# Optimization experiments

Measured on AMD Instinct MI355X. Metric: run time of the kernel, lower is better.

Reference implementation:

```python
import jax, jax.numpy as jnp
import numpy as np

N_NODES = 100000
N_EDGES = 1600000
HIDDEN = 128
N_GRAPHS = 64
N_CLASSES = 10


def setup_inputs() -> dict:
    key = jax.random.key(0)
    ks = jax.random.split(key, 10)
    x = jax.random.normal(ks[0], (N_NODES, 1), dtype=jnp.float32)
    edge_index = jax.random.randint(ks[1], (2, N_EDGES), 0, N_NODES, dtype=jnp.int32)
    batch = jnp.sort(jax.random.randint(ks[2], (N_NODES,), 0, N_GRAPHS, dtype=jnp.int32))
    def glorot(k, shape):
        fan_in, fan_out = shape
        s = jnp.sqrt(6.0 / (fan_in + fan_out))
        return jax.random.uniform(k, shape, jnp.float32, -s, s)
    return {
        "x": x,
        "edge_index": edge_index,
        "batch": batch,
        "W1l": glorot(ks[3], (1, HIDDEN)),
        "W1r": glorot(ks[4], (1, HIDDEN)),
        "b1": jnp.zeros((HIDDEN,), jnp.float32),
        "W2l": glorot(ks[5], (HIDDEN, HIDDEN)),
        "W2r": glorot(ks[6], (HIDDEN, HIDDEN)),
        "b2": jnp.zeros((HIDDEN,), jnp.float32),
        "W3l": glorot(ks[7], (HIDDEN, HIDDEN)),
        "W3r": glorot(ks[8], (HIDDEN, HIDDEN)),
        "b3": jnp.zeros((HIDDEN,), jnp.float32),
        "Wfc": glorot(ks[9], (HIDDEN, N_CLASSES)),
        "bfc": jnp.zeros((N_CLASSES,), jnp.float32),
    }


def _sage_conv(x, src, dst, Wl, Wr, b, n_nodes):
    # mean aggregation of source features at destination nodes
    msg = x[src]                                              # [E, d_in]
    agg = jax.ops.segment_sum(msg, dst, num_segments=n_nodes)  # [N, d_in]
    cnt = jax.ops.segment_sum(jnp.ones((src.shape[0], 1), x.dtype), dst,
                              num_segments=n_nodes)            # [N, 1]
    mean = agg / jnp.maximum(cnt, 1.0)
    # PyG SAGEConv: lin_l(mean neighbors) + bias + lin_r(self)
    return mean @ Wl + b + x @ Wr


def reference(x, edge_index, batch, W1l, W1r, b1, W2l, W2r, b2,
              W3l, W3r, b3, Wfc, bfc):
    src, dst = edge_index[0], edge_index[1]
    n = x.shape[0]
    h = jax.nn.relu(_sage_conv(x, src, dst, W1l, W1r, b1, n))
    h = jax.nn.relu(_sage_conv(h, src, dst, W2l, W2r, b2, n))
    h = jax.nn.relu(_sage_conv(h, src, dst, W3l, W3r, b3, n))
    # global_mean_pool over graph ids in `batch`
    pooled = jax.ops.segment_sum(h, batch, num_segments=N_GRAPHS)
    gcnt = jax.ops.segment_sum(jnp.ones((n, 1), h.dtype), batch,
                               num_segments=N_GRAPHS)
    pooled = pooled / jnp.maximum(gcnt, 1.0)
    logits = pooled @ Wfc + bfc
    return jax.nn.log_softmax(logits, axis=1)
```

## Files before the change

kernel.cpp:

```cpp
#include <hip/hip_runtime.h>

typedef unsigned int u32;
typedef unsigned short u16;
typedef short bf16x8 __attribute__((ext_vector_type(8)));
typedef float f32x4 __attribute__((ext_vector_type(4)));
typedef float f32x2 __attribute__((ext_vector_type(2)));
typedef u32 u32x4 __attribute__((ext_vector_type(4)));

#define HBLK 256

__device__ __forceinline__ u16 f2bf(float f) {
  u32 u = __float_as_uint(f);
  u = (u + 0x7FFFu + ((u >> 16) & 1u)) >> 16;
  return (u16)u;
}
__device__ __forceinline__ float bf2f(u32 h) { return __uint_as_float(h << 16); }

__global__ void hist_wprep_kernel(const int* __restrict__ dst, int* __restrict__ boff,
                                  int* __restrict__ btotal, int E, int nbuk, int chunk,
                                  const float* __restrict__ W2l, const float* __restrict__ W2r,
                                  const float* __restrict__ W3l, const float* __restrict__ W3r,
                                  u16* __restrict__ wt2, u16* __restrict__ wt3,
                                  float* __restrict__ pooled, int* __restrict__ gcnt) {
  int idx = blockIdx.x * 256 + threadIdx.x;
  {
    int which = idx >> 15, r = idx & 32767;
    int j = r >> 8, k = r & 255;
    if (which == 0) {
      float v = (k < 128) ? W2l[k * 128 + j] : W2r[(k - 128) * 128 + j];
      wt2[r] = f2bf(v);
    } else {
      float v = (k < 128) ? W3l[k * 128 + j] : W3r[(k - 128) * 128 + j];
      wt3[r] = f2bf(v);
    }
    if (idx < 8192) pooled[idx] = 0.f;
    if (idx < 64) gcnt[idx] = 0;
  }
  __shared__ int h[1024];
  for (int i = threadIdx.x; i < nbuk; i += 256) h[i] = 0;
  __syncthreads();
  int b0 = blockIdx.x * chunk, b1 = min(b0 + chunk, E);
  for (int e = b0 + threadIdx.x; e < b1; e += 256)
    atomicAdd(&h[dst[e] >> 7], 1);
  __syncthreads();
  for (int i = threadIdx.x; i < nbuk; i += 256)
    boff[i * HBLK + blockIdx.x] = atomicAdd(&btotal[i], h[i]);
}

__global__ void scatter2_kernel(const int* __restrict__ src, const int* __restrict__ dst,
                                const int* __restrict__ btotal, const int* __restrict__ boff,
                                u32* __restrict__ part, int* __restrict__ bbase,
                                int E, int nbuk, int chunk) {
  __shared__ int bt[1024];
  __shared__ int wsum[256];
  __shared__ int cur[1024];
  int tid = threadIdx.x;
  int t4 = tid * 4;
  int v0 = (t4 + 0 < nbuk) ? btotal[t4 + 0] : 0;
  int v1 = (t4 + 1 < nbuk) ? btotal[t4 + 1] : 0;
  int v2 = (t4 + 2 < nbuk) ? btotal[t4 + 2] : 0;
  int v3 = (t4 + 3 < nbuk) ? btotal[t4 + 3] : 0;
  int sum = v0 + v1 + v2 + v3;
  wsum[tid] = sum;
  __syncthreads();
  for (int off = 1; off < 256; off <<= 1) {
    int t = (tid >= off) ? wsum[tid - off] : 0;
    __syncthreads();
    wsum[tid] += t;
    __syncthreads();
  }
  int excl = wsum[tid] - sum;
  bt[t4 + 0] = excl;
  bt[t4 + 1] = excl + v0;
  bt[t4 + 2] = excl + v0 + v1;
  bt[t4 + 3] = excl + v0 + v1 + v2;
  __syncthreads();
  for (int i = tid; i < nbuk; i += 256) {
    cur[i] = bt[i] + boff[i * HBLK + blockIdx.x];
    if (blockIdx.x == 0) bbase[i] = bt[i];
  }
  __syncthreads();
  int b0 = blockIdx.x * chunk, b1 = min(b0 + chunk, E);
  for (int e = b0 + tid; e < b1; e += 256) {
    int d = dst[e];
    int pos = atomicAdd(&cur[d >> 7], 1);
    part[pos] = (u32)src[e] | ((u32)(d & 127) << 25);
  }
}

__global__ void scatter3_kernel(const u32* __restrict__ part, const int* __restrict__ bbase,
                                const float* __restrict__ x,
                                const float* __restrict__ W1l, const float* __restrict__ W1r,
                                const float* __restrict__ b1,
                                int* __restrict__ roff, int* __restrict__ csr,
                                u32* __restrict__ h1, int E, int nbuk, int n) {
  int b = blockIdx.x;
  int tid = threadIdx.x;
  int base = bbase[b];
  int end = (b + 1 < nbuk) ? bbase[b + 1] : E;
  __shared__ int cnt[128];
  __shared__ int s[128];
  __shared__ int cur[128];
  __shared__ float xsum[128];
  __shared__ float meanv[128];
  __shared__ float wlA[128], wrA[128], bA[128];
  if (tid < 128) {
    cnt[tid] = 0; xsum[tid] = 0.f;
    wlA[tid] = W1l[tid]; wrA[tid] = W1r[tid]; bA[tid] = b1[tid];
  }
  __syncthreads();
  for (int e = base + tid; e < end; e += 256)
    atomicAdd(&cnt[part[e] >> 25], 1);
  __syncthreads();
  if (tid < 128) s[tid] = cnt[tid];
  __syncthreads();
  for (int off = 1; off < 128; off <<= 1) {
    int t = (tid >= off && tid < 128) ? s[tid - off] : 0;
    __syncthreads();
    if (tid < 128) s[tid] += t;
    __syncthreads();
  }
  if (tid < 128) {
    int excl = s[tid] - cnt[tid];
    cur[tid] = base + excl;
    int node = b * 128 + tid;
    if (node < n) roff[node] = base + excl;
  }
  if (b == 0 && tid == 0) roff[n] = E;
  __syncthreads();
  for (int e = base + tid; e < end; e += 256) {
    u32 p = part[e];
    int sidx = (int)(p & 0x1FFFFFFu);
    int pos = atomicAdd(&cur[p >> 25], 1);
    csr[pos] = sidx;
    atomicAdd(&xsum[p >> 25], x[sidx]);
  }
  __syncthreads();
  if (tid < 128) meanv[tid] = xsum[tid] / (float)max(cnt[tid], 1);
  __syncthreads();
  int nlocal = min(128, n - b * 128);
  for (int q = tid; q < nlocal * 64; q += 256) {
    int ln = q >> 6, w = q & 63;
    int node = b * 128 + ln;
    int j0 = w * 2;
    float m = meanv[ln], xs = x[node];
    float v0 = fmaxf(m * wlA[j0] + xs * wrA[j0] + bA[j0], 0.f);
    float v1 = fmaxf(m * wlA[j0 + 1] + xs * wrA[j0 + 1] + bA[j0 + 1], 0.f);
    h1[(size_t)node * 64 + w] = (u32)f2bf(v0) | ((u32)f2bf(v1) << 16);
  }
}

__device__ __forceinline__ u32x4 grow(const u32* hp, int s) {
  return *(const u32x4*)(hp + (size_t)s * 64);
}
__device__ __forceinline__ void acc_row(f32x2* a, u32x4 v) {
#pragma unroll
  for (int w = 0; w < 4; ++w)
    a[w] += (f32x2){bf2f(v[w] & 0xFFFFu), bf2f(v[w] >> 16)};
}

__global__ void agg_kernel(const int* __restrict__ csr, const int* __restrict__ roff,
                           const u32* __restrict__ hin, u32* __restrict__ outv, int n) {
  int g = threadIdx.x >> 4, li = threadIdx.x & 15;
  int i = blockIdx.x * 16 + g;
  if (i >= n) return;
  int e0 = roff[i], e1 = roff[i + 1];
  f32x2 a[4] = {};
  const u32* hp = hin + li * 4;
  int e = e0;
  for (; e + 7 < e1; e += 8) {
    int s0 = csr[e], s1 = csr[e + 1], s2 = csr[e + 2], s3 = csr[e + 3];
    int s4 = csr[e + 4], s5 = csr[e + 5], s6 = csr[e + 6], s7 = csr[e + 7];
    u32x4 v0 = grow(hp, s0), v1 = grow(hp, s1), v2 = grow(hp, s2), v3 = grow(hp, s3);
    u32x4 v4 = grow(hp, s4), v5 = grow(hp, s5), v6 = grow(hp, s6), v7 = grow(hp, s7);
    acc_row(a, v0); acc_row(a, v1); acc_row(a, v2); acc_row(a, v3);
    acc_row(a, v4); acc_row(a, v5); acc_row(a, v6); acc_row(a, v7);
  }
  for (; e + 3 < e1; e += 4) {
    int s0 = csr[e], s1 = csr[e + 1], s2 = csr[e + 2], s3 = csr[e + 3];
    u32x4 v0 = grow(hp, s0), v1 = grow(hp, s1), v2 = grow(hp, s2), v3 = grow(hp, s3);
    acc_row(a, v0); acc_row(a, v1); acc_row(a, v2); acc_row(a, v3);
  }
  for (; e < e1; ++e) acc_row(a, grow(hp, csr[e]));
  float inv = 1.f / (float)max(e1 - e0, 1);
  u32x4 o;
#pragma unroll
  for (int w = 0; w < 4; ++w)
    o[w] = (u32)f2bf(a[w].x * inv) | ((u32)f2bf(a[w].y * inv) << 16);
  *(u32x4*)(outv + (size_t)i * 64 + li * 4) = o;
}

__launch_bounds__(512)
__global__ void mm_kernel(const u16* Aleft, const u16* Aright,
                          const u16* __restrict__ Wt, const float* __restrict__ bias,
                          u16* Out, int n) {
  __shared__ u16 wlds[32768];
  for (int c = threadIdx.x; c < 4096; c += 512) {
    int j = c >> 5, ch = c & 31;
    int swz = ch ^ (j & 31);
    *(u32x4*)(&wlds[j * 256 + swz * 8]) = *(const u32x4*)(&Wt[j * 256 + ch * 8]);
  }
  __syncthreads();
  int wave = threadIdx.x >> 6;
  int lane = threadIdx.x & 63;
  int quad = lane >> 4, l16 = lane & 15;
  int row0 = blockIdx.x * 128 + wave * 16;
  int m = row0 + l16;
  int mc = m < n ? m : (n - 1);
  f32x4 acc[8] = {};
  const u16* Ah[2] = {Aleft, Aright};
#pragma unroll
  for (int half = 0; half < 2; ++half) {
    const u16* A = Ah[half] + (size_t)mc * 128;
#pragma unroll
    for (int s = 0; s < 4; ++s) {
      bf16x8 a = *(const bf16x8*)(A + s * 32 + quad * 8);
      int chunk = (half << 4) + (s << 2) + quad;
#pragma unroll
      for (int t = 0; t < 8; ++t) {
        int j = t * 16 + l16;
        int swz = chunk ^ (j & 31);
        bf16x8 b = *(const bf16x8*)(&wlds[j * 256 + swz * 8]);
        acc[t] = __builtin_amdgcn_mfma_f32_16x16x32_bf16(a, b, acc[t], 0, 0, 0);
      }
    }
  }
  __syncthreads();
  int rl_base = wave * 16 + quad * 4;
#pragma unroll
  for (int t = 0; t < 8; ++t) {
    int j = t * 16 + l16;
    float bj = bias[j];
#pragma unroll
    for (int r = 0; r < 4; ++r) {
      float v = acc[t][r] + bj;
      wlds[(rl_base + r) * 136 + j] = f2bf(fmaxf(v, 0.f));
    }
  }
  __syncthreads();
  int base_row = blockIdx.x * 128;
  for (int q = 0; q < 4; ++q) {
    int idx = q * 512 + threadIdx.x;
    int rl = idx >> 4;
    int ch = idx & 15;
    int mr = base_row + rl;
    if (mr < n)
      *(u32x4*)(&Out[(size_t)mr * 128 + ch * 8]) =
          *(const u32x4*)(&wlds[rl * 136 + ch * 8]);
  }
}

#define PB_NODES 128
__global__ void pool_partial(const int* __restrict__ batch, const u32* __restrict__ h3,
                             float* __restrict__ pooled, int* __restrict__ gcnt, int n) {
  __shared__ int bg[PB_NODES];
  int tid = threadIdx.x;
  int start = blockIdx.x * PB_NODES;
  int cntN = min(PB_NODES, n - start);
  if (tid < cntN) bg[tid] = batch[start + tid];
  __syncthreads();
  int wave = tid >> 6, lane = tid & 63;
  float a0 = 0.f, a1 = 0.f;
  int gcur = -1, cnt = 0;
  int k = wave;
  for (; k + 12 < cntN; k += 16) {
    u32 v0 = h3[(size_t)(start + k) * 64 + lane];
    u32 v1 = h3[(size_t)(start + k + 4) * 64 + lane];
    u32 v2 = h3[(size_t)(start + k + 8) * 64 + lane];
    u32 v3 = h3[(size_t)(start + k + 12) * 64 + lane];
    int g0 = bg[k], g1 = bg[k + 4], g2 = bg[k + 8], g3 = bg[k + 12];
    u32 vv[4] = {v0, v1, v2, v3};
    int gg[4] = {g0, g1, g2, g3};
#pragma unroll
    for (int q = 0; q < 4; ++q) {
      if (gg[q] != gcur) {
        if (gcur >= 0) {
          atomicAdd(&pooled[gcur * 128 + lane * 2], a0);
          atomicAdd(&pooled[gcur * 128 + lane * 2 + 1], a1);
          if (lane == 0) atomicAdd(&gcnt[gcur], cnt);
        }
        gcur = gg[q]; a0 = 0.f; a1 = 0.f; cnt = 0;
      }
      a0 += bf2f(vv[q] & 0xFFFFu);
      a1 += bf2f(vv[q] >> 16);
      cnt++;
    }
  }
  for (; k < cntN; k += 4) {
    u32 v = h3[(size_t)(start + k) * 64 + lane];
    int g = bg[k];
    if (g != gcur) {
      if (gcur >= 0) {
        atomicAdd(&pooled[gcur * 128 + lane * 2], a0);
        atomicAdd(&pooled[gcur * 128 + lane * 2 + 1], a1);
        if (lane == 0) atomicAdd(&gcnt[gcur], cnt);
      }
      gcur = g; a0 = 0.f; a1 = 0.f; cnt = 0;
    }
    a0 += bf2f(v & 0xFFFFu);
    a1 += bf2f(v >> 16);
    cnt++;
  }
  if (gcur >= 0) {
    atomicAdd(&pooled[gcur * 128 + lane * 2], a0);
    atomicAdd(&pooled[gcur * 128 + lane * 2 + 1], a1);
    if (lane == 0) atomicAdd(&gcnt[gcur], cnt);
  }
}

__global__ void head_kernel(const float* __restrict__ pooled, const int* __restrict__ gcnt,
                            const float* __restrict__ Wfc, const float* __restrict__ bfc,
                            float* __restrict__ out) {
  __shared__ float lg[64][10];
  int t = threadIdx.x;
  if (t < 640) {
    int g = t / 10, c = t % 10;
    float inv = 1.f / (float)max(gcnt[g], 1);
    float acc = bfc[c];
    for (int k = 0; k < 128; ++k) acc += pooled[g * 128 + k] * inv * Wfc[k * 10 + c];
    lg[g][c] = acc;
  }
  __syncthreads();
  if (t < 640) {
    int g = t / 10, c = t % 10;
    float mx = -1e30f;
    for (int q = 0; q < 10; ++q) mx = fmaxf(mx, lg[g][q]);
    float se = 0.f;
    for (int q = 0; q < 10; ++q) se += expf(lg[g][q] - mx);
    out[g * 10 + c] = lg[g][c] - mx - logf(se);
  }
}

extern "C" void kernel_launch(void* const* d_in, const int* in_sizes, int n_in,
                              void* d_out, int out_size, void* d_ws, size_t ws_size,
                              hipStream_t stream) {
  const float* x   = (const float*)d_in[0];
  const int* ei    = (const int*)d_in[1];
  const int* batch = (const int*)d_in[2];
  const float* W1l = (const float*)d_in[3];
  const float* W1r = (const float*)d_in[4];
  const float* b1  = (const float*)d_in[5];
  const float* W2l = (const float*)d_in[6];
  const float* W2r = (const float*)d_in[7];
  const float* b2  = (const float*)d_in[8];
  const float* W3l = (const float*)d_in[9];
  const float* W3r = (const float*)d_in[10];
  const float* b3  = (const float*)d_in[11];
  const float* Wfc = (const float*)d_in[12];
  const float* bfc = (const float*)d_in[13];
  float* out = (float*)d_out;
  int N = in_sizes[0];
  int E = in_sizes[1] / 2;
  const int* src = ei;
  const int* dst = ei + E;

  char* p = (char*)d_ws;
  auto alloc = [&](size_t bytes) { void* r = (void*)p; p += (bytes + 255) & ~(size_t)255; return r; };
  int* roff   = (int*)alloc((size_t)(N + 1) * 4);
  int* csr    = (int*)alloc((size_t)E * 4);
  u32* bufA   = (u32*)alloc((size_t)N * 64 * 4);
  u32* bufB   = (u32*)alloc((size_t)N * 64 * 4);
  u16* wt2    = (u16*)alloc(32768 * 2);
  u16* wt3    = (u16*)alloc(32768 * 2);
  float* pooled = (float*)alloc(64 * 128 * 4);
  int* gcnt   = (int*)alloc(64 * 4);
  int* btotal = (int*)alloc(1024 * 4);
  int* bbase  = (int*)alloc(1024 * 4);

  int nbuk = (N + 127) >> 7;
  int* boff = (int*)bufA;
  u32* part = (u32*)bufB;
  int chunk = (E + HBLK - 1) / HBLK;

  hipMemsetAsync(btotal, 0, 1024 * 4, stream);
  hist_wprep_kernel<<<HBLK, 256, 0, stream>>>(dst, boff, btotal, E, nbuk, chunk,
                                              W2l, W2r, W3l, W3r, wt2, wt3,
                                              pooled, gcnt);
  scatter2_kernel<<<HBLK, 256, 0, stream>>>(src, dst, btotal, boff, part, bbase,
                                            E, nbuk, chunk);
  scatter3_kernel<<<nbuk, 256, 0, stream>>>(part, bbase, x, W1l, W1r, b1,
                                            roff, csr, bufA, E, nbuk, N);
  agg_kernel<<<(N + 15) / 16, 256, 0, stream>>>(csr, roff, bufA, bufB, N);
  mm_kernel<<<(N + 127) / 128, 512, 0, stream>>>((const u16*)bufB, (const u16*)bufA, wt2, b2,
                                                 (u16*)bufB, N);
  agg_kernel<<<(N + 15) / 16, 256, 0, stream>>>(csr, roff, bufB, bufA, N);
  mm_kernel<<<(N + 127) / 128, 512, 0, stream>>>((const u16*)bufA, (const u16*)bufB, wt3, b3,
                                                 (u16*)bufA, N);
  pool_partial<<<(N + PB_NODES - 1) / PB_NODES, 256, 0, stream>>>(batch, bufA, pooled, gcnt, N);
  head_kernel<<<1, 640, 0, stream>>>(pooled, gcnt, Wfc, bfc, out);
}
```

Measured before the change: 332.0 us.

## Fuse neighbor aggregation with SAGE matmul and pooling into one kernel

Combines the gather-mean aggregation and the MFMA linear layer into one kernel per layer. The aggregated rows now stay in LDS instead of going out to and back from global memory. The last layer also does the global mean pooling straight from the LDS output tile, so h3 is never written and pool_partial is gone. Graph node counts move into the histogram kernel and one memset now zeroes pooled, gcnt and btotal together. The cost is a large LDS footprint (about 80KB per 256-thread block), which limits occupancy for the latency-bound gather phase, and the gather and MFMA phases now run in series within each block.

```diff
diff --git a/kernel.cpp b/kernel.cpp
--- a/kernel.cpp
+++ b/kernel.cpp
@@ -21,7 +21,7 @@
                                   const float* __restrict__ W2l, const float* __restrict__ W2r,
                                   const float* __restrict__ W3l, const float* __restrict__ W3r,
                                   u16* __restrict__ wt2, u16* __restrict__ wt3,
-                                  float* __restrict__ pooled, int* __restrict__ gcnt) {
+                                  const int* __restrict__ batch, int* __restrict__ gcnt, int n) {
   int idx = blockIdx.x * 256 + threadIdx.x;
   {
     int which = idx >> 15, r = idx & 32767;
@@ -33,18 +33,24 @@
       float v = (k < 128) ? W3l[k * 128 + j] : W3r[(k - 128) * 128 + j];
       wt3[r] = f2bf(v);
     }
-    if (idx < 8192) pooled[idx] = 0.f;
-    if (idx < 64) gcnt[idx] = 0;
   }
   __shared__ int h[1024];
+  __shared__ int gh[64];
   for (int i = threadIdx.x; i < nbuk; i += 256) h[i] = 0;
+  if (threadIdx.x < 64) gh[threadIdx.x] = 0;
   __syncthreads();
   int b0 = blockIdx.x * chunk, b1 = min(b0 + chunk, E);
   for (int e = b0 + threadIdx.x; e < b1; e += 256)
     atomicAdd(&h[dst[e] >> 7], 1);
+  int chunkN = (n + HBLK - 1) / HBLK;
+  int n0 = blockIdx.x * chunkN, n1 = min(n0 + chunkN, n);
+  for (int i = n0 + threadIdx.x; i < n1; i += 256)
+    atomicAdd(&gh[batch[i]], 1);
   __syncthreads();
   for (int i = threadIdx.x; i < nbuk; i += 256)
     boff[i * HBLK + blockIdx.x] = atomicAdd(&btotal[i], h[i]);
+  if (threadIdx.x < 64 && gh[threadIdx.x] > 0)
+    atomicAdd(&gcnt[threadIdx.x], gh[threadIdx.x]);
 }
 
 __global__ void scatter2_kernel(const int* __restrict__ src, const int* __restrict__ dst,
@@ -159,70 +165,86 @@
     a[w] += (f32x2){bf2f(v[w] & 0xFFFFu), bf2f(v[w] >> 16)};
 }
 
-__global__ void agg_kernel(const int* __restrict__ csr, const int* __restrict__ roff,
-                           const u32* __restrict__ hin, u32* __restrict__ outv, int n) {
-  int g = threadIdx.x >> 4, li = threadIdx.x & 15;
-  int i = blockIdx.x * 16 + g;
-  if (i >= n) return;
-  int e0 = roff[i], e1 = roff[i + 1];
-  f32x2 a[4] = {};
-  const u32* hp = hin + li * 4;
-  int e = e0;
-  for (; e + 7 < e1; e += 8) {
-    int s0 = csr[e], s1 = csr[e + 1], s2 = csr[e + 2], s3 = csr[e + 3];
-    int s4 = csr[e + 4], s5 = csr[e + 5], s6 = csr[e + 6], s7 = csr[e + 7];
-    u32x4 v0 = grow(hp, s0), v1 = grow(hp, s1), v2 = grow(hp, s2), v3 = grow(hp, s3);
-    u32x4 v4 = grow(hp, s4), v5 = grow(hp, s5), v6 = grow(hp, s6), v7 = grow(hp, s7);
-    acc_row(a, v0); acc_row(a, v1); acc_row(a, v2); acc_row(a, v3);
-    acc_row(a, v4); acc_row(a, v5); acc_row(a, v6); acc_row(a, v7);
-  }
-  for (; e + 3 < e1; e += 4) {
-    int s0 = csr[e], s1 = csr[e + 1], s2 = csr[e + 2], s3 = csr[e + 3];
-    u32x4 v0 = grow(hp, s0), v1 = grow(hp, s1), v2 = grow(hp, s2), v3 = grow(hp, s3);
-    acc_row(a, v0); acc_row(a, v1); acc_row(a, v2); acc_row(a, v3);
-  }
-  for (; e < e1; ++e) acc_row(a, grow(hp, csr[e]));
-  float inv = 1.f / (float)max(e1 - e0, 1);
-  u32x4 o;
-#pragma unroll
-  for (int w = 0; w < 4; ++w)
-    o[w] = (u32)f2bf(a[w].x * inv) | ((u32)f2bf(a[w].y * inv) << 16);
-  *(u32x4*)(outv + (size_t)i * 64 + li * 4) = o;
-}
-
-__launch_bounds__(512)
-__global__ void mm_kernel(const u16* Aleft, const u16* Aright,
-                          const u16* __restrict__ Wt, const float* __restrict__ bias,
-                          u16* Out, int n) {
+template <int MODE>
+__launch_bounds__(256, 2)
+__global__ void fused_aggmm(const int* __restrict__ csr, const int* __restrict__ roff,
+                            const u32* __restrict__ hin,
+                            const u16* __restrict__ Wt, const float* __restrict__ bias,
+                            u16* __restrict__ Out,
+                            const int* __restrict__ batch, float* __restrict__ pooled,
+                            int n) {
   __shared__ u16 wlds[32768];
-  for (int c = threadIdx.x; c < 4096; c += 512) {
+  __shared__ u16 mlds[8192];
+  int tid = threadIdx.x;
+  for (int c = tid; c < 4096; c += 256) {
     int j = c >> 5, ch = c & 31;
     int swz = ch ^ (j & 31);
     *(u32x4*)(&wlds[j * 256 + swz * 8]) = *(const u32x4*)(&Wt[j * 256 + ch * 8]);
   }
-  __syncthreads();
-  int wave = threadIdx.x >> 6;
-  int lane = threadIdx.x & 63;
+  int g = tid >> 4, li = tid & 15;
+  const u32* hp = hin + li * 4;
+  for (int q = 0; q < 4; ++q) {
+    int lr = g * 4 + q;
+    int i = blockIdx.x * 64 + lr;
+    u32x4 o = {0u, 0u, 0u, 0u};
+    if (i < n) {
+      int e0 = roff[i], e1 = roff[i + 1];
+      f32x2 a[4] = {};
+      int e = e0;
+      for (; e + 7 < e1; e += 8) {
+        int s0 = csr[e], s1 = csr[e + 1], s2 = csr[e + 2], s3 = csr[e + 3];
+        int s4 = csr[e + 4], s5 = csr[e + 5], s6 = csr[e + 6], s7 = csr[e + 7];
+        u32x4 v0 = grow(hp, s0), v1 = grow(hp, s1), v2 = grow(hp, s2), v3 = grow(hp, s3);
+        u32x4 v4 = grow(hp, s4), v5 = grow(hp, s5), v6 = grow(hp, s6), v7 = grow(hp, s7);
+        acc_row(a, v0); acc_row(a, v1); acc_row(a, v2); acc_row(a, v3);
+        acc_row(a, v4); acc_row(a, v5); acc_row(a, v6); acc_row(a, v7);
+      }
+      for (; e + 3 < e1; e += 4) {
+        int s0 = csr[e], s1 = csr[e + 1], s2 = csr[e + 2], s3 = csr[e + 3];
+        u32x4 v0 = grow(hp, s0), v1 = grow(hp, s1), v2 = grow(hp, s2), v3 = grow(hp, s3);
+        acc_row(a, v0); acc_row(a, v1); acc_row(a, v2); acc_row(a, v3);
+      }
+      for (; e < e1; ++e) acc_row(a, grow(hp, csr[e]));
+      float inv = 1.f / (float)max(e1 - e0, 1);
+#pragma unroll
+      for (int w = 0; w < 4; ++w)
+        o[w] = (u32)f2bf(a[w].x * inv) | ((u32)f2bf(a[w].y * inv) << 16);
+    }
+    int swz = li ^ (lr & 15);
+    *(u32x4*)(&mlds[lr * 128 + swz * 8]) = o;
+  }
+  __syncthreads();
+  int wave = tid >> 6, lane = tid & 63;
   int quad = lane >> 4, l16 = lane & 15;
-  int row0 = blockIdx.x * 128 + wave * 16;
-  int m = row0 + l16;
+  int lr0 = wave * 16;
+  int m = blockIdx.x * 64 + lr0 + l16;
   int mc = m < n ? m : (n - 1);
   f32x4 acc[8] = {};
-  const u16* Ah[2] = {Aleft, Aright};
-#pragma unroll
-  for (int half = 0; half < 2; ++half) {
-    const u16* A = Ah[half] + (size_t)mc * 128;
-#pragma unroll
-    for (int s = 0; s < 4; ++s) {
-      bf16x8 a = *(const bf16x8*)(A + s * 32 + quad * 8);
-      int chunk = (half << 4) + (s << 2) + quad;
-#pragma unroll
-      for (int t = 0; t < 8; ++t) {
-        int j = t * 16 + l16;
-        int swz = chunk ^ (j & 31);
-        bf16x8 b = *(const bf16x8*)(&wlds[j * 256 + swz * 8]);
-        acc[t] = __builtin_amdgcn_mfma_f32_16x16x32_bf16(a, b, acc[t], 0, 0, 0);
-      }
+#pragma unroll
+  for (int s = 0; s < 4; ++s) {
+    int lrr = lr0 + l16;
+    int c = s * 4 + quad;
+    bf16x8 a = *(const bf16x8*)(&mlds[lrr * 128 + (c ^ (lrr & 15)) * 8]);
+    int chunk = s * 4 + quad;
+#pragma unroll
+    for (int t = 0; t < 8; ++t) {
+      int j = t * 16 + l16;
+      int swz = chunk ^ (j & 31);
+      bf16x8 b = *(const bf16x8*)(&wlds[j * 256 + swz * 8]);
+      acc[t] = __builtin_amdgcn_mfma_f32_16x16x32_bf16(a, b, acc[t], 0, 0, 0);
+    }
+  }
+  const u16* A = (const u16*)hin + (size_t)mc * 128;
+#pragma unroll
+  for (int s = 0; s < 4; ++s) {
+    bf16x8 a = *(const bf16x8*)(A + s * 32 + quad * 8);
+    int chunk = 16 + s * 4 + quad;
+#pragma unroll
+    for (int t = 0; t < 8; ++t) {
+      int j = t * 16 + l16;
+      int swz = chunk ^ (j & 31);
+      bf16x8 b = *(const bf16x8*)(&wlds[j * 256 + swz * 8]);
+      acc[t] = __builtin_amdgcn_mfma_f32_16x16x32_bf16(a, b, acc[t], 0, 0, 0);
     }
   }
   __syncthreads();
@@ -237,74 +259,40 @@
       wlds[(rl_base + r) * 136 + j] = f2bf(fmaxf(v, 0.f));
     }
   }
-  __syncthreads();
-  int base_row = blockIdx.x * 128;
-  for (int q = 0; q < 4; ++q) {
-    int idx = q * 512 + threadIdx.x;
-    int rl = idx >> 4;
-    int ch = idx & 15;
-    int mr = base_row + rl;
-    if (mr < n)
-      *(u32x4*)(&Out[(size_t)mr * 128 + ch * 8]) =
-          *(const u32x4*)(&wlds[rl * 136 + ch * 8]);
-  }
-}
-
-#define PB_NODES 128
-__global__ void pool_partial(const int* __restrict__ batch, const u32* __restrict__ h3,
-                             float* __restrict__ pooled, int* __restrict__ gcnt, int n) {
-  __shared__ int bg[PB_NODES];
-  int tid = threadIdx.x;
-  int start = blockIdx.x * PB_NODES;
-  int cntN = min(PB_NODES, n - start);
-  if (tid < cntN) bg[tid] = batch[start + tid];
-  __syncthreads();
-  int wave = tid >> 6, lane = tid & 63;
-  float a0 = 0.f, a1 = 0.f;
-  int gcur = -1, cnt = 0;
-  int k = wave;
-  for (; k + 12 < cntN; k += 16) {
-    u32 v0 = h3[(size_t)(start + k) * 64 + lane];
-    u32 v1 = h3[(size_t)(start + k + 4) * 64 + lane];
-    u32 v2 = h3[(size_t)(start + k + 8) * 64 + lane];
-    u32 v3 = h3[(size_t)(start + k + 12) * 64 + lane];
-    int g0 = bg[k], g1 = bg[k + 4], g2 = bg[k + 8], g3 = bg[k + 12];
-    u32 vv[4] = {v0, v1, v2, v3};
-    int gg[4] = {g0, g1, g2, g3};
-#pragma unroll
-    for (int q = 0; q < 4; ++q) {
-      if (gg[q] != gcur) {
-        if (gcur >= 0) {
-          atomicAdd(&pooled[gcur * 128 + lane * 2], a0);
-          atomicAdd(&pooled[gcur * 128 + lane * 2 + 1], a1);
-          if (lane == 0) atomicAdd(&gcnt[gcur], cnt);
-        }
-        gcur = gg[q]; a0 = 0.f; a1 = 0.f; cnt = 0;
+  if (MODE == 1) {
+    int* bgp = (int*)mlds;
+    if (tid < 64) {
+      int rr = blockIdx.x * 64 + tid;
+      bgp[tid] = (rr < n) ? batch[rr] : -1;
+    }
+  }
+  __syncthreads();
+  if (MODE == 0) {
+    int base_row = blockIdx.x * 64;
+    for (int qq = 0; qq < 4; ++qq) {
+      int idx = qq * 256 + tid;
+      int rl = idx >> 4;
+      int ch = idx & 15;
+      int mr = base_row + rl;
+      if (mr < n)
+        *(u32x4*)(&Out[(size_t)mr * 128 + ch * 8]) =
+            *(const u32x4*)(&wlds[rl * 136 + ch * 8]);
+    }
+  } else {
+    const int* bgp = (const int*)mlds;
+    int tcol = tid & 127, half = tid >> 7;
+    float accp = 0.f;
+    int gcur = -1;
+    for (int r = half * 32; r < half * 32 + 32; ++r) {
+      int gb = bgp[r];
+      if (gb != gcur) {
+        if (gcur >= 0) atomicAdd(&pooled[gcur * 128 + tcol], accp);
+        gcur = gb;
+        accp = 0.f;
       }
-      a0 += bf2f(vv[q] & 0xFFFFu);
-      a1 += bf2f(vv[q] >> 16);
-      cnt++;
-    }
-  }
-  for (; k < cntN; k += 4) {
-    u32 v = h3[(size_t)(start + k) * 64 + lane];
-    int g = bg[k];
-    if (g != gcur) {
-      if (gcur >= 0) {
-        atomicAdd(&pooled[gcur * 128 + lane * 2], a0);
-        atomicAdd(&pooled[gcur * 128 + lane * 2 + 1], a1);
-        if (lane == 0) atomicAdd(&gcnt[gcur], cnt);
-      }
-      gcur = g; a0 = 0.f; a1 = 0.f; cnt = 0;
-    }
-    a0 += bf2f(v & 0xFFFFu);
-    a1 += bf2f(v >> 16);
-    cnt++;
-  }
-  if (gcur >= 0) {
-    atomicAdd(&pooled[gcur * 128 + lane * 2], a0);
-    atomicAdd(&pooled[gcur * 128 + lane * 2 + 1], a1);
-    if (lane == 0) atomicAdd(&gcnt[gcur], cnt);
+      if (gb >= 0) accp += bf2f((u32)wlds[r * 136 + tcol]);
+    }
+    if (gcur >= 0) atomicAdd(&pooled[gcur * 128 + tcol], accp);
   }
 }
 
@@ -372,20 +360,18 @@
   u32* part = (u32*)bufB;
   int chunk = (E + HBLK - 1) / HBLK;
 
-  hipMemsetAsync(btotal, 0, 1024 * 4, stream);
+  hipMemsetAsync(pooled, 0, 32768 + 256 + 4096, stream);
   hist_wprep_kernel<<<HBLK, 256, 0, stream>>>(dst, boff, btotal, E, nbuk, chunk,
                                               W2l, W2r, W3l, W3r, wt2, wt3,
-                                              pooled, gcnt);
+                                              batch, gcnt, N);
   scatter2_kernel<<<HBLK, 256, 0, stream>>>(src, dst, btotal, boff, part, bbase,
                                             E, nbuk, chunk);
   scatter3_kernel<<<nbuk, 256, 0, stream>>>(part, bbase, x, W1l, W1r, b1,
                                             roff, csr, bufA, E, nbuk, N);
-  agg_kernel<<<(N + 15) / 16, 256, 0, stream>>>(csr, roff, bufA, bufB, N);
-  mm_kernel<<<(N + 127) / 128, 512, 0, stream>>>((const u16*)bufB, (const u16*)bufA, wt2, b2,
-                                                 (u16*)bufB, N);
-  agg_kernel<<<(N + 15) / 16, 256, 0, stream>>>(csr, roff, bufB, bufA, N);
-  mm_kernel<<<(N + 127) / 128, 512, 0, stream>>>((const u16*)bufA, (const u16*)bufB, wt3, b3,
-                                                 (u16*)bufA, N);
-  pool_partial<<<(N + PB_NODES - 1) / PB_NODES, 256, 0, stream>>>(batch, bufA, pooled, gcnt, N);
+  int fgrid = (N + 63) / 64;
+  fused_aggmm<0><<<fgrid, 256, 0, stream>>>(csr, roff, bufA, wt2, b2,
+                                            (u16*)bufB, batch, pooled, N);
+  fused_aggmm<1><<<fgrid, 256, 0, stream>>>(csr, roff, bufB, wt3, b3,
+                                            (u16*)bufA, batch, pooled, N);
   head_kernel<<<1, 640, 0, stream>>>(pooled, gcnt, Wfc, bfc, out);
 }
```

New measurement: 393.7 us. 18.6% more time.
